# Kernel optimization log

Hardware: AMD Instinct MI355X
Metric: run time of the kernel (lower is better)

Reference implementation:

```python
import jax, jax.numpy as jnp
import numpy as np

EPS = 1e-5

def _bn(x, gamma, beta):
    # BatchNorm1d training-mode math: batch mean / biased variance over edge dim
    mean = jnp.mean(x, axis=0)
    var = jnp.mean(jnp.square(x - mean), axis=0)
    return (x - mean) * (gamma / jnp.sqrt(var + EPS)) + beta


def setup_inputs() -> dict:
    key = jax.random.key(0)
    ks = jax.random.split(key, 12)
    n, d, s, h, e = 50000, 256, 32, 128, 500000
    feat = 3 * d + s + 1  # 801
    sc = lambda fan_in: 1.0 / np.sqrt(fan_in)
    return {
        "node_embeddings": jax.random.normal(ks[0], (n, d), jnp.float32),
        "gradient_scores": jax.random.normal(ks[1], (e,), jnp.float32),
        "step_embedding": jax.random.normal(ks[2], (s,), jnp.float32),
        "W1": jax.random.normal(ks[3], (feat, h), jnp.float32) * sc(feat),
        "b1": jnp.zeros((h,), jnp.float32),
        "g1": jnp.ones((h,), jnp.float32),
        "be1": jnp.zeros((h,), jnp.float32),
        "W2": jax.random.normal(ks[4], (h, h // 2), jnp.float32) * sc(h),
        "b2": jnp.zeros((h // 2,), jnp.float32),
        "g2": jnp.ones((h // 2,), jnp.float32),
        "be2": jnp.zeros((h // 2,), jnp.float32),
        "W3": jax.random.normal(ks[5], (h // 2, 1), jnp.float32) * sc(h // 2),
        "b3": jnp.zeros((1,), jnp.float32),
        "edge_index": jax.random.randint(ks[6], (2, e), 0, n, jnp.int64),
    }


def reference(node_embeddings, gradient_scores, step_embedding,
              W1, b1, g1, be1, W2, b2, g2, be2, W3, b3, edge_index):
    src, dst = edge_index[0], edge_index[1]
    h_u = node_embeddings[src]              # [E, d]
    h_v = node_embeddings[dst]              # [E, d]
    edge_diff = jnp.abs(h_u - h_v)          # [E, d]
    E = edge_index.shape[1]
    step = jnp.broadcast_to(step_embedding[None, :], (E, step_embedding.shape[0]))
    feats = jnp.concatenate([h_u, h_v, edge_diff, step, gradient_scores[:, None]], axis=1)
    x = jnp.maximum(feats @ W1 + b1, 0.0)
    x = _bn(x, g1, be1)                     # dropout is identity in eval
    x = jnp.maximum(x @ W2 + b2, 0.0)
    x = _bn(x, g2, be2)
    out = jnp.tanh(x @ W3 + b3)[:, 0]       # [E]
    return out
```

## Files before the change

### kernel.cpp

```cpp
#include <hip/hip_runtime.h>

#define NE 500000
#define DIMK 256
#define H1 128
#define H2 64
#define EPSBN 1e-5f
#define NT1 977
#define GRID2 1024
#define NJOBS2 1954

typedef _Float16 half8 __attribute__((ext_vector_type(8)));
typedef float f32x4 __attribute__((ext_vector_type(4)));
typedef unsigned short ushort8 __attribute__((ext_vector_type(8)));

static __device__ __forceinline__ half8 habs8(half8 x) {
  ushort8 u = __builtin_bit_cast(ushort8, x);
  u &= (unsigned short)0x7FFF;
  return __builtin_bit_cast(half8, u);
}
static __device__ __forceinline__ float h2f(unsigned int u) {
  return (float)__builtin_bit_cast(_Float16, (unsigned short)(u & 0xffff));
}

__global__ void k_prep(const float* __restrict__ W1, const float* __restrict__ b1,
                       const float* __restrict__ step, float* __restrict__ c0) {
  const int j = threadIdx.x;
  if (j < H1) {
    float a = b1[j];
#pragma unroll
    for (int tt = 0; tt < 32; ++tt) a += step[tt] * W1[(768 + tt) * H1 + j];
    c0[j] = a;
  }
}

__global__ void k_prep16(const float* __restrict__ emb, _Float16* __restrict__ embh) {
  const int i = (blockIdx.x * 256 + threadIdx.x) * 8;
  const float4 a = *(const float4*)(emb + i);
  const float4 b = *(const float4*)(emb + i + 4);
  half8 h;
  h[0] = (_Float16)a.x; h[1] = (_Float16)a.y; h[2] = (_Float16)a.z; h[3] = (_Float16)a.w;
  h[4] = (_Float16)b.x; h[5] = (_Float16)b.y; h[6] = (_Float16)b.z; h[7] = (_Float16)b.w;
  *(half8*)(embh + i) = h;
}

__global__ void k_prepB(const float* __restrict__ W1, _Float16* __restrict__ bfrag) {
  const int g = blockIdx.x * 256 + threadIdx.x;
  const int lane = g & 63, f = g >> 6;
  const int c = f & 7, kc = (f >> 3) & 7, s = f >> 6;
  const int row0 = s * 256 + kc * 32 + (lane >> 4) * 8;
  const int col = c * 16 + (lane & 15);
  half8 h;
#pragma unroll
  for (int j = 0; j < 8; ++j) h[j] = (_Float16)W1[(row0 + j) * H1 + col];
  *(half8*)(bfrag + (size_t)g * 8) = h;
}

__global__ __launch_bounds__(1024, 4)
void k_layer1(const _Float16* __restrict__ embh, const void* __restrict__ eidx_raw,
              const float* __restrict__ grad, const float* __restrict__ W1,
              const float* __restrict__ c0, const _Float16* __restrict__ bfrag,
              _Float16* __restrict__ x1, float* __restrict__ p1) {
  __shared__ __align__(16) _Float16 ldsB[49152];
  __shared__ int s_src[512], s_dst[512];
  __shared__ float s_g[512];
  __shared__ float s_wg[64], s_c0[64], s_sum[64], s_sq[64];

  const int t = threadIdx.x, bid = blockIdx.x;
  const int ch = bid & 1;
  const int w = t >> 6, lane = t & 63, quad = lane >> 4, m15 = lane & 15;

  {
    const half8* gb = (const half8*)bfrag;
    half8* lb = (half8*)ldsB;
    for (int i = t; i < 6144; i += 1024) {
      const int li = i & 63, fl = i >> 6;
      const int c = fl & 3, kc = (fl >> 2) & 7, s = fl >> 5;
      lb[i] = gb[(size_t)((s * 64 + kc * 8 + ch * 4 + c) * 64 + li)];
    }
  }
  if (t < 64) {
    s_wg[t] = W1[800 * H1 + ch * 64 + t];
    s_c0[t] = c0[ch * 64 + t];
    s_sum[t] = 0.f; s_sq[t] = 0.f;
  }

  const unsigned* ew = (const unsigned*)eidx_raw;
  const bool is64 = ((ew[1] | ew[3] | ew[5] | ew[7]) == 0u);
  const int* e32 = (const int*)eidx_raw;
  const long long* e64 = (const long long*)eidx_raw;

  float st_s[4] = {0, 0, 0, 0}, st_q[4] = {0, 0, 0, 0};
  const half8* lb = (const half8*)ldsB;

  for (int tile = (bid >> 1); tile < NT1; tile += 128) {
    const int base = tile * 512;
    __syncthreads();
    if (t < 512) {
      int e = base + t; if (e >= NE) e = NE - 1;
      if (is64) { s_src[t] = (int)e64[e]; s_dst[t] = (int)e64[NE + e]; }
      else      { s_src[t] = e32[e];      s_dst[t] = e32[NE + e]; }
      s_g[t] = grad[e];
    }
    __syncthreads();

    const int row0 = w * 32 + m15;
    const _Float16* pu0 = embh + (size_t)s_src[row0] * DIMK + quad * 8;
    const _Float16* pv0 = embh + (size_t)s_dst[row0] * DIMK + quad * 8;
    const _Float16* pu1 = embh + (size_t)s_src[row0 + 16] * DIMK + quad * 8;
    const _Float16* pv1 = embh + (size_t)s_dst[row0 + 16] * DIMK + quad * 8;

    f32x4 acc[2][4];
#pragma unroll
    for (int r = 0; r < 2; ++r)
#pragma unroll
      for (int c = 0; c < 4; ++c) acc[r][c] = (f32x4)0.f;

#pragma unroll 1
    for (int kc = 0; kc < 8; ++kc) {
      const half8 u0 = *(const half8*)(pu0 + kc * 32);
      const half8 v0 = *(const half8*)(pv0 + kc * 32);
      const half8 u1 = *(const half8*)(pu1 + kc * 32);
      const half8 v1 = *(const half8*)(pv1 + kc * 32);
      const half8 d0 = habs8(u0 - v0);
      const half8 d1 = habs8(u1 - v1);
#pragma unroll
      for (int c = 0; c < 4; ++c) {
        const half8 bu = lb[((0 * 8 + kc) * 4 + c) * 64 + lane];
        const half8 bv = lb[((1 * 8 + kc) * 4 + c) * 64 + lane];
        const half8 bd = lb[((2 * 8 + kc) * 4 + c) * 64 + lane];
        acc[0][c] = __builtin_amdgcn_mfma_f32_16x16x32_f16(u0, bu, acc[0][c], 0, 0, 0);
        acc[1][c] = __builtin_amdgcn_mfma_f32_16x16x32_f16(u1, bu, acc[1][c], 0, 0, 0);
        acc[0][c] = __builtin_amdgcn_mfma_f32_16x16x32_f16(v0, bv, acc[0][c], 0, 0, 0);
        acc[1][c] = __builtin_amdgcn_mfma_f32_16x16x32_f16(v1, bv, acc[1][c], 0, 0, 0);
        acc[0][c] = __builtin_amdgcn_mfma_f32_16x16x32_f16(d0, bd, acc[0][c], 0, 0, 0);
        acc[1][c] = __builtin_amdgcn_mfma_f32_16x16x32_f16(d1, bd, acc[1][c], 0, 0, 0);
      }
    }
#pragma unroll
    for (int r = 0; r < 2; ++r) {
      const int rrow = w * 32 + r * 16 + quad * 4;
#pragma unroll
      for (int c = 0; c < 4; ++c) {
        const int colL = c * 16 + m15;
        const float wgv = s_wg[colL], c0v = s_c0[colL];
#pragma unroll
        for (int reg = 0; reg < 4; ++reg) {
          const int e = base + rrow + reg;
          float x = acc[r][c][reg] + s_g[rrow + reg] * wgv + c0v;
          x = fmaxf(x, 0.f);
          if (e >= NE) x = 0.f;
          st_s[c] += x; st_q[c] += x * x;
          if (e < NE) x1[(size_t)e * H1 + ch * 64 + colL] = (_Float16)x;
        }
      }
    }
  }
  __syncthreads();
#pragma unroll
  for (int c = 0; c < 4; ++c) {
    float a = st_s[c]; a += __shfl_xor(a, 16); a += __shfl_xor(a, 32);
    float b = st_q[c]; b += __shfl_xor(b, 16); b += __shfl_xor(b, 32);
    if (lane < 16) { atomicAdd(&s_sum[c * 16 + m15], a); atomicAdd(&s_sq[c * 16 + m15], b); }
  }
  __syncthreads();
  if (t < 64) {
    const int colG = ch * 64 + t, bh = bid >> 1;
    p1[colG * 128 + bh] = s_sum[t];
    p1[128 * 128 + colG * 128 + bh] = s_sq[t];
  }
}

__global__ void k_fin1(const float* __restrict__ p1, const float* __restrict__ g1,
                       const float* __restrict__ be1, const float* __restrict__ W2,
                       const float* __restrict__ b2, float* __restrict__ w2f,
                       float* __restrict__ b2f) {
  __shared__ float s1[128], t1[128];
  const int t = threadIdx.x;
  if (t < 128) {
    float s = 0.f, q = 0.f;
    const float4* rs = (const float4*)(p1 + t * 128);
    const float4* rq = (const float4*)(p1 + 128 * 128 + t * 128);
#pragma unroll 4
    for (int i = 0; i < 32; ++i) {
      float4 a = rs[i]; s += a.x + a.y + a.z + a.w;
      float4 b = rq[i]; q += b.x + b.y + b.z + b.w;
    }
    const float inv = 1.0f / (float)NE;
    float mean = s * inv;
    float var = q * inv - mean * mean;
    float sc = g1[t] * rsqrtf(var + EPSBN);
    s1[t] = sc; t1[t] = be1[t] - mean * sc;
  }
  __syncthreads();
  for (int i = t; i < H1 * H2; i += 256) w2f[i] = s1[i >> 6] * W2[i];
  if (t < 64) {
    float b = b2[t];
    for (int j = 0; j < 128; ++j) b += t1[j] * W2[j * 64 + t];
    b2f[t] = b;
  }
}

__global__ __launch_bounds__(256, 2)
void k_layer2(const _Float16* __restrict__ x1, const float* __restrict__ w2f,
              const float* __restrict__ b2f, _Float16* __restrict__ x2,
              float* __restrict__ p2) {
  __shared__ __align__(16) _Float16 b_lds[8192];
  __shared__ float s_b[64], s_sum[64], s_sq[64];
  const int t = threadIdx.x, bid = blockIdx.x;
  const int w = t >> 6, lane = t & 63, quad = lane >> 4, m15 = lane & 15;

  for (int i = t; i < 8192; i += 256) {
    const int j = i & 7, li = (i >> 3) & 63, f = i >> 9;
    const int c = f & 3, kk = f >> 2;
    const int row = kk * 32 + (li >> 4) * 8 + j;
    const int col = c * 16 + (li & 15);
    b_lds[i] = (_Float16)w2f[row * H2 + col];
  }
  if (t < 64) { s_b[t] = b2f[t]; s_sum[t] = 0.f; s_sq[t] = 0.f; }
  __syncthreads();

  float st_s[4] = {0, 0, 0, 0}, st_q[4] = {0, 0, 0, 0};
  const half8* bp = (const half8*)b_lds;

  for (int job = bid; job < NJOBS2; job += GRID2) {
    const int base = job * 256;
    const _Float16* pa[4];
#pragma unroll
    for (int r = 0; r < 4; ++r) {
      int e = base + w * 64 + r * 16 + m15; if (e >= NE) e = NE - 1;
      pa[r] = x1 + (size_t)e * H1 + quad * 8;
    }
    f32x4 acc[4][4];
#pragma unroll
    for (int r = 0; r < 4; ++r)
#pragma unroll
      for (int c = 0; c < 4; ++c) acc[r][c] = (f32x4)0.f;

#pragma unroll
    for (int kk = 0; kk < 4; ++kk) {
      half8 a[4];
#pragma unroll
      for (int r = 0; r < 4; ++r) a[r] = *(const half8*)(pa[r] + kk * 32);
#pragma unroll
      for (int c = 0; c < 4; ++c) {
        const half8 bf = bp[(kk * 4 + c) * 64 + lane];
#pragma unroll
        for (int r = 0; r < 4; ++r)
          acc[r][c] = __builtin_amdgcn_mfma_f32_16x16x32_f16(a[r], bf, acc[r][c], 0, 0, 0);
      }
    }
#pragma unroll
    for (int r = 0; r < 4; ++r) {
      const int erow = w * 64 + r * 16 + quad * 4;
#pragma unroll
      for (int c = 0; c < 4; ++c) {
        const int colL = c * 16 + m15;
        const float bv = s_b[colL];
#pragma unroll
        for (int reg = 0; reg < 4; ++reg) {
          const int e = base + erow + reg;
          float x = acc[r][c][reg] + bv;
          x = fmaxf(x, 0.f);
          if (e >= NE) x = 0.f;
          st_s[c] += x; st_q[c] += x * x;
          if (e < NE) x2[(size_t)e * H2 + colL] = (_Float16)x;
        }
      }
    }
  }
  __syncthreads();
#pragma unroll
  for (int c = 0; c < 4; ++c) {
    float a = st_s[c]; a += __shfl_xor(a, 16); a += __shfl_xor(a, 32);
    float b = st_q[c]; b += __shfl_xor(b, 16); b += __shfl_xor(b, 32);
    if (lane < 16) { atomicAdd(&s_sum[c * 16 + m15], a); atomicAdd(&s_sq[c * 16 + m15], b); }
  }
  __syncthreads();
  if (t < 64) {
    p2[t * GRID2 + bid] = s_sum[t];
    p2[64 * GRID2 + t * GRID2 + bid] = s_sq[t];
  }
}

__global__ void k_fin2(const float* __restrict__ p2, const float* __restrict__ g2,
                       const float* __restrict__ be2, const float* __restrict__ W3,
                       const float* __restrict__ b3, float* __restrict__ w3f,
                       float* __restrict__ b3f) {
  __shared__ float tp[64];
  const int t = threadIdx.x;
  if (t < 64) {
    float s = 0.f, q = 0.f;
    const float4* rs = (const float4*)(p2 + t * GRID2);
    const float4* rq = (const float4*)(p2 + 64 * GRID2 + t * GRID2);
#pragma unroll 4
    for (int i = 0; i < GRID2 / 4; ++i) {
      float4 a = rs[i]; s += a.x + a.y + a.z + a.w;
      float4 b = rq[i]; q += b.x + b.y + b.z + b.w;
    }
    const float inv = 1.0f / (float)NE;
    float mean = s * inv;
    float var = q * inv - mean * mean;
    float sc = g2[t] * rsqrtf(var + EPSBN);
    float tt = be2[t] - mean * sc;
    w3f[t] = sc * W3[t];
    tp[t] = tt * W3[t];
  }
  __syncthreads();
  if (t == 0) {
    float b = b3[0];
    for (int j = 0; j < 64; ++j) b += tp[j];
    b3f[0] = b;
  }
}

__global__ __launch_bounds__(256)
void k_out(const unsigned short* __restrict__ x2, const float* __restrict__ w3f,
           const float* __restrict__ b3f, float* __restrict__ out) {
  __shared__ float s_w[64];
  __shared__ float s_b;
  const int t = threadIdx.x;
  if (t < 64) s_w[t] = w3f[t];
  if (t == 0) s_b = b3f[0];
  __syncthreads();
  const int gid = blockIdx.x * 256 + t;
  const int e = gid >> 2, p = gid & 3;
  if (e < NE) {
    const uint4* r = (const uint4*)(x2 + (size_t)e * H2 + p * 16);
    float s = 0.f;
#pragma unroll
    for (int i = 0; i < 2; ++i) {
      const uint4 u = r[i];
      const int jb = p * 16 + i * 8;
      s += h2f(u.x) * s_w[jb + 0] + h2f(u.x >> 16) * s_w[jb + 1];
      s += h2f(u.y) * s_w[jb + 2] + h2f(u.y >> 16) * s_w[jb + 3];
      s += h2f(u.z) * s_w[jb + 4] + h2f(u.z >> 16) * s_w[jb + 5];
      s += h2f(u.w) * s_w[jb + 6] + h2f(u.w >> 16) * s_w[jb + 7];
    }
    s += __shfl_xor(s, 1);
    s += __shfl_xor(s, 2);
    if (p == 0) out[e] = tanhf(s + s_b);
  }
}

extern "C" void kernel_launch(void* const* d_in, const int* in_sizes, int n_in,
                              void* d_out, int out_size, void* d_ws, size_t ws_size,
                              hipStream_t stream) {
  const float* emb  = (const float*)d_in[0];
  const float* grad = (const float*)d_in[1];
  const float* step = (const float*)d_in[2];
  const float* W1   = (const float*)d_in[3];
  const float* b1   = (const float*)d_in[4];
  const float* g1   = (const float*)d_in[5];
  const float* be1  = (const float*)d_in[6];
  const float* W2   = (const float*)d_in[7];
  const float* b2   = (const float*)d_in[8];
  const float* g2   = (const float*)d_in[9];
  const float* be2  = (const float*)d_in[10];
  const float* W3   = (const float*)d_in[11];
  const float* b3   = (const float*)d_in[12];
  const void*  eidx = (const void*)d_in[13];
  float* out = (float*)d_out;

  char* ws = (char*)d_ws;
  _Float16* embh  = (_Float16*)(ws + 0);
  _Float16* x2    = (_Float16*)(ws + 0);
  _Float16* bfrag = (_Float16*)(ws + 25600000LL);
  float*    c0    = (float*)(ws + 25796608LL);
  _Float16* x1    = (_Float16*)(ws + 64000000LL);
  float* p1  = (float*)(ws + 192000000LL);
  float* p2  = (float*)(ws + 192131072LL);
  float* w2f = (float*)(ws + 192655360LL);
  float* b2f = (float*)(ws + 192688128LL);
  float* w3f = (float*)(ws + 192688384LL);
  float* b3f = (float*)(ws + 192688640LL);

  k_prep  <<<1,    256, 0, stream>>>(W1, b1, step, c0);
  k_prep16<<<6250, 256, 0, stream>>>(emb, embh);
  k_prepB <<<48,   256, 0, stream>>>(W1, bfrag);
  k_layer1<<<256, 1024, 0, stream>>>(embh, eidx, grad, W1, c0, bfrag, x1, p1);
  k_fin1  <<<1,    256, 0, stream>>>(p1, g1, be1, W2, b2, w2f, b2f);
  k_layer2<<<GRID2,256, 0, stream>>>(x1, w2f, b2f, x2, p2);
  k_fin2  <<<1,    128, 0, stream>>>(p2, g2, be2, W3, b3, w3f, b3f);
  k_out   <<<7813, 256, 0, stream>>>((const unsigned short*)x2, w3f, b3f, out);
}
```

Before: 405.5 us.

## Restructure layer1 into small blocks reading W1 fragments from global with prefetch

Layer 1 now runs 768 blocks of 256 threads, each computing all 128 output columns for a 128-edge tile, instead of 256 blocks of 1024 threads split across two column halves. The 96KB LDS staging of the weight fragments is removed, so B fragments are read from global memory (expected to hit in cache), and the gathered embeddings for the next k-chunk are prefetched into registers. This avoids gathering each edge's embeddings twice and allows higher occupancy, but puts weight reads on the global/L2 path and roughly doubles accumulator registers. Layer 2 launch bounds are also raised to 4 blocks.

```diff
diff --git a/kernel.cpp b/kernel.cpp
--- a/kernel.cpp
+++ b/kernel.cpp
@@ -5,9 +5,10 @@
 #define H1 128
 #define H2 64
 #define EPSBN 1e-5f
-#define NT1 977
-#define GRID2 1024
-#define NJOBS2 1954
+#define GE1 768
+#define NT1 3907
+#define G2 1024
+#define NT2 1954
 
 typedef _Float16 half8 __attribute__((ext_vector_type(8)));
 typedef float f32x4 __attribute__((ext_vector_type(4)));
@@ -55,32 +56,21 @@
   *(half8*)(bfrag + (size_t)g * 8) = h;
 }
 
-__global__ __launch_bounds__(1024, 4)
+__global__ __launch_bounds__(256, 3)
 void k_layer1(const _Float16* __restrict__ embh, const void* __restrict__ eidx_raw,
               const float* __restrict__ grad, const float* __restrict__ W1,
               const float* __restrict__ c0, const _Float16* __restrict__ bfrag,
               _Float16* __restrict__ x1, float* __restrict__ p1) {
-  __shared__ __align__(16) _Float16 ldsB[49152];
-  __shared__ int s_src[512], s_dst[512];
-  __shared__ float s_g[512];
-  __shared__ float s_wg[64], s_c0[64], s_sum[64], s_sq[64];
+  __shared__ int s_src[128], s_dst[128];
+  __shared__ float s_g[128];
+  __shared__ float s_wg[128], s_c0[128], s_sum[128], s_sq[128];
 
   const int t = threadIdx.x, bid = blockIdx.x;
-  const int ch = bid & 1;
   const int w = t >> 6, lane = t & 63, quad = lane >> 4, m15 = lane & 15;
 
-  {
-    const half8* gb = (const half8*)bfrag;
-    half8* lb = (half8*)ldsB;
-    for (int i = t; i < 6144; i += 1024) {
-      const int li = i & 63, fl = i >> 6;
-      const int c = fl & 3, kc = (fl >> 2) & 7, s = fl >> 5;
-      lb[i] = gb[(size_t)((s * 64 + kc * 8 + ch * 4 + c) * 64 + li)];
-    }
-  }
-  if (t < 64) {
-    s_wg[t] = W1[800 * H1 + ch * 64 + t];
-    s_c0[t] = c0[ch * 64 + t];
+  if (t < 128) {
+    s_wg[t] = W1[800 * H1 + t];
+    s_c0[t] = c0[t];
     s_sum[t] = 0.f; s_sq[t] = 0.f;
   }
 
@@ -89,13 +79,13 @@
   const int* e32 = (const int*)eidx_raw;
   const long long* e64 = (const long long*)eidx_raw;
 
-  float st_s[4] = {0, 0, 0, 0}, st_q[4] = {0, 0, 0, 0};
-  const half8* lb = (const half8*)ldsB;
-
-  for (int tile = (bid >> 1); tile < NT1; tile += 128) {
-    const int base = tile * 512;
+  float st_s[8] = {0, 0, 0, 0, 0, 0, 0, 0}, st_q[8] = {0, 0, 0, 0, 0, 0, 0, 0};
+  const half8* bp = (const half8*)bfrag;
+
+  for (int tile = bid; tile < NT1; tile += GE1) {
+    const int base = tile * 128;
     __syncthreads();
-    if (t < 512) {
+    if (t < 128) {
       int e = base + t; if (e >= NE) e = NE - 1;
       if (is64) { s_src[t] = (int)e64[e]; s_dst[t] = (int)e64[NE + e]; }
       else      { s_src[t] = e32[e];      s_dst[t] = e32[NE + e]; }
@@ -109,25 +99,33 @@
     const _Float16* pu1 = embh + (size_t)s_src[row0 + 16] * DIMK + quad * 8;
     const _Float16* pv1 = embh + (size_t)s_dst[row0 + 16] * DIMK + quad * 8;
 
-    f32x4 acc[2][4];
+    f32x4 acc[2][8];
 #pragma unroll
     for (int r = 0; r < 2; ++r)
 #pragma unroll
-      for (int c = 0; c < 4; ++c) acc[r][c] = (f32x4)0.f;
+      for (int c = 0; c < 8; ++c) acc[r][c] = (f32x4)0.f;
+
+    half8 u0 = *(const half8*)pu0;
+    half8 v0 = *(const half8*)pv0;
+    half8 u1 = *(const half8*)pu1;
+    half8 v1 = *(const half8*)pv1;
 
 #pragma unroll 1
     for (int kc = 0; kc < 8; ++kc) {
-      const half8 u0 = *(const half8*)(pu0 + kc * 32);
-      const half8 v0 = *(const half8*)(pv0 + kc * 32);
-      const half8 u1 = *(const half8*)(pu1 + kc * 32);
-      const half8 v1 = *(const half8*)(pv1 + kc * 32);
+      half8 nu0, nv0, nu1, nv1;
+      if (kc < 7) {
+        nu0 = *(const half8*)(pu0 + (kc + 1) * 32);
+        nv0 = *(const half8*)(pv0 + (kc + 1) * 32);
+        nu1 = *(const half8*)(pu1 + (kc + 1) * 32);
+        nv1 = *(const half8*)(pv1 + (kc + 1) * 32);
+      }
       const half8 d0 = habs8(u0 - v0);
       const half8 d1 = habs8(u1 - v1);
 #pragma unroll
-      for (int c = 0; c < 4; ++c) {
-        const half8 bu = lb[((0 * 8 + kc) * 4 + c) * 64 + lane];
-        const half8 bv = lb[((1 * 8 + kc) * 4 + c) * 64 + lane];
-        const half8 bd = lb[((2 * 8 + kc) * 4 + c) * 64 + lane];
+      for (int c = 0; c < 8; ++c) {
+        const half8 bu = bp[(kc * 8 + c) * 64 + lane];
+        const half8 bv = bp[(64 + kc * 8 + c) * 64 + lane];
+        const half8 bd = bp[(128 + kc * 8 + c) * 64 + lane];
         acc[0][c] = __builtin_amdgcn_mfma_f32_16x16x32_f16(u0, bu, acc[0][c], 0, 0, 0);
         acc[1][c] = __builtin_amdgcn_mfma_f32_16x16x32_f16(u1, bu, acc[1][c], 0, 0, 0);
         acc[0][c] = __builtin_amdgcn_mfma_f32_16x16x32_f16(v0, bv, acc[0][c], 0, 0, 0);
@@ -135,38 +133,38 @@
         acc[0][c] = __builtin_amdgcn_mfma_f32_16x16x32_f16(d0, bd, acc[0][c], 0, 0, 0);
         acc[1][c] = __builtin_amdgcn_mfma_f32_16x16x32_f16(d1, bd, acc[1][c], 0, 0, 0);
       }
+      if (kc < 7) { u0 = nu0; v0 = nv0; u1 = nu1; v1 = nv1; }
     }
 #pragma unroll
     for (int r = 0; r < 2; ++r) {
-      const int rrow = w * 32 + r * 16 + quad * 4;
-#pragma unroll
-      for (int c = 0; c < 4; ++c) {
+      const int erow = w * 32 + r * 16 + quad * 4;
+#pragma unroll
+      for (int c = 0; c < 8; ++c) {
         const int colL = c * 16 + m15;
         const float wgv = s_wg[colL], c0v = s_c0[colL];
 #pragma unroll
         for (int reg = 0; reg < 4; ++reg) {
-          const int e = base + rrow + reg;
-          float x = acc[r][c][reg] + s_g[rrow + reg] * wgv + c0v;
+          const int e = base + erow + reg;
+          float x = acc[r][c][reg] + s_g[erow + reg] * wgv + c0v;
           x = fmaxf(x, 0.f);
           if (e >= NE) x = 0.f;
           st_s[c] += x; st_q[c] += x * x;
-          if (e < NE) x1[(size_t)e * H1 + ch * 64 + colL] = (_Float16)x;
+          if (e < NE) x1[(size_t)e * H1 + colL] = (_Float16)x;
         }
       }
     }
   }
   __syncthreads();
 #pragma unroll
-  for (int c = 0; c < 4; ++c) {
+  for (int c = 0; c < 8; ++c) {
     float a = st_s[c]; a += __shfl_xor(a, 16); a += __shfl_xor(a, 32);
     float b = st_q[c]; b += __shfl_xor(b, 16); b += __shfl_xor(b, 32);
     if (lane < 16) { atomicAdd(&s_sum[c * 16 + m15], a); atomicAdd(&s_sq[c * 16 + m15], b); }
   }
   __syncthreads();
-  if (t < 64) {
-    const int colG = ch * 64 + t, bh = bid >> 1;
-    p1[colG * 128 + bh] = s_sum[t];
-    p1[128 * 128 + colG * 128 + bh] = s_sq[t];
+  if (t < 128) {
+    p1[t * GE1 + bid] = s_sum[t];
+    p1[128 * GE1 + t * GE1 + bid] = s_sq[t];
   }
 }
 
@@ -178,10 +176,10 @@
   const int t = threadIdx.x;
   if (t < 128) {
     float s = 0.f, q = 0.f;
-    const float4* rs = (const float4*)(p1 + t * 128);
-    const float4* rq = (const float4*)(p1 + 128 * 128 + t * 128);
+    const float4* rs = (const float4*)(p1 + t * GE1);
+    const float4* rq = (const float4*)(p1 + 128 * GE1 + t * GE1);
 #pragma unroll 4
-    for (int i = 0; i < 32; ++i) {
+    for (int i = 0; i < GE1 / 4; ++i) {
       float4 a = rs[i]; s += a.x + a.y + a.z + a.w;
       float4 b = rq[i]; q += b.x + b.y + b.z + b.w;
     }
@@ -200,7 +198,7 @@
   }
 }
 
-__global__ __launch_bounds__(256, 2)
+__global__ __launch_bounds__(256, 4)
 void k_layer2(const _Float16* __restrict__ x1, const float* __restrict__ w2f,
               const float* __restrict__ b2f, _Float16* __restrict__ x2,
               float* __restrict__ p2) {
@@ -222,7 +220,7 @@
   float st_s[4] = {0, 0, 0, 0}, st_q[4] = {0, 0, 0, 0};
   const half8* bp = (const half8*)b_lds;
 
-  for (int job = bid; job < NJOBS2; job += GRID2) {
+  for (int job = bid; job < NT2; job += G2) {
     const int base = job * 256;
     const _Float16* pa[4];
 #pragma unroll
@@ -277,8 +275,8 @@
   }
   __syncthreads();
   if (t < 64) {
-    p2[t * GRID2 + bid] = s_sum[t];
-    p2[64 * GRID2 + t * GRID2 + bid] = s_sq[t];
+    p2[t * G2 + bid] = s_sum[t];
+    p2[64 * G2 + t * G2 + bid] = s_sq[t];
   }
 }
 
@@ -290,10 +288,10 @@
   const int t = threadIdx.x;
   if (t < 64) {
     float s = 0.f, q = 0.f;
-    const float4* rs = (const float4*)(p2 + t * GRID2);
-    const float4* rq = (const float4*)(p2 + 64 * GRID2 + t * GRID2);
+    const float4* rs = (const float4*)(p2 + t * G2);
+    const float4* rq = (const float4*)(p2 + 64 * G2 + t * G2);
 #pragma unroll 4
-    for (int i = 0; i < GRID2 / 4; ++i) {
+    for (int i = 0; i < G2 / 4; ++i) {
       float4 a = rs[i]; s += a.x + a.y + a.z + a.w;
       float4 b = rq[i]; q += b.x + b.y + b.z + b.w;
     }
@@ -366,20 +364,20 @@
   _Float16* x2    = (_Float16*)(ws + 0);
   _Float16* bfrag = (_Float16*)(ws + 25600000LL);
   float*    c0    = (float*)(ws + 25796608LL);
+  float*    p1    = (float*)(ws + 30000000LL);
   _Float16* x1    = (_Float16*)(ws + 64000000LL);
-  float* p1  = (float*)(ws + 192000000LL);
-  float* p2  = (float*)(ws + 192131072LL);
-  float* w2f = (float*)(ws + 192655360LL);
-  float* b2f = (float*)(ws + 192688128LL);
-  float* w3f = (float*)(ws + 192688384LL);
-  float* b3f = (float*)(ws + 192688640LL);
-
-  k_prep  <<<1,    256, 0, stream>>>(W1, b1, step, c0);
-  k_prep16<<<6250, 256, 0, stream>>>(emb, embh);
-  k_prepB <<<48,   256, 0, stream>>>(W1, bfrag);
-  k_layer1<<<256, 1024, 0, stream>>>(embh, eidx, grad, W1, c0, bfrag, x1, p1);
-  k_fin1  <<<1,    256, 0, stream>>>(p1, g1, be1, W2, b2, w2f, b2f);
-  k_layer2<<<GRID2,256, 0, stream>>>(x1, w2f, b2f, x2, p2);
-  k_fin2  <<<1,    128, 0, stream>>>(p2, g2, be2, W3, b3, w3f, b3f);
-  k_out   <<<7813, 256, 0, stream>>>((const unsigned short*)x2, w3f, b3f, out);
-}
+  float*    p2    = (float*)(ws + 192000000LL);
+  float*    w2f   = (float*)(ws + 192524288LL);
+  float*    b2f   = (float*)(ws + 192557056LL);
+  float*    w3f   = (float*)(ws + 192557312LL);
+  float*    b3f   = (float*)(ws + 192557568LL);
+
+  k_prep   <<<1,    256, 0, stream>>>(W1, b1, step, c0);
+  k_prep16 <<<6250, 256, 0, stream>>>(emb, embh);
+  k_prepB  <<<48,   256, 0, stream>>>(W1, bfrag);
+  k_layer1 <<<GE1,  256, 0, stream>>>(embh, eidx, grad, W1, c0, bfrag, x1, p1);
+  k_fin1   <<<1,    256, 0, stream>>>(p1, g1, be1, W2, b2, w2f, b2f);
+  k_layer2 <<<G2,   256, 0, stream>>>(x1, w2f, b2f, x2, p2);
+  k_fin2   <<<1,    128, 0, stream>>>(p2, g2, be2, W3, b3, w3f, b3f);
+  k_out    <<<7813, 256, 0, stream>>>((const unsigned short*)x2, w3f, b3f, out);
+}
```

After: 506.8 us. 25.0% more time.
